# Kernel tuning notes

Measured on AMD Instinct MI355X. Metric: run time of the kernel, lower is better.

The kernel has to match this reference:

```python
import jax, jax.numpy as jnp
import numpy as np
import math

N_HEADS = 16
HEAD_SIZE = 64
N_EMBED = 1024


def setup_inputs() -> dict:
    key = jax.random.key(0)
    ks = jax.random.split(key, 5)
    B, T, C = 2, 2048, N_EMBED
    s = 0.02
    return {
        "x": jax.random.normal(ks[0], (B, T, C), dtype=jnp.float32),
        "c_attn_w": jax.random.normal(ks[1], (C, 3 * C), dtype=jnp.float32) * s,
        "c_attn_b": jax.random.normal(ks[2], (3 * C,), dtype=jnp.float32) * s,
        "c_proj_w": jax.random.normal(ks[3], (C, C), dtype=jnp.float32) * s,
        "c_proj_b": jax.random.normal(ks[4], (C,), dtype=jnp.float32) * s,
    }


def reference(x, c_attn_w, c_attn_b, c_proj_w, c_proj_b):
    B, T, C = x.shape
    H, D = N_HEADS, HEAD_SIZE
    kqv = x @ c_attn_w + c_attn_b                      # [B,T,3C]
    k, q, v = jnp.split(kqv, 3, axis=-1)               # source split order: k, q, v
    k = k.reshape(B, T, H, D).transpose(0, 2, 1, 3)    # [B,H,T,D]
    q = q.reshape(B, T, H, D).transpose(0, 2, 1, 3)
    v = v.reshape(B, T, H, D).transpose(0, 2, 1, 3)
    # NOTE: faithful to source: scores = K @ Q^T (not Q @ K^T)
    wei = jnp.einsum("bhid,bhjd->bhij", k, q) * (1.0 / math.sqrt(D))
    causal = jnp.tril(jnp.ones((T, T), dtype=bool))    # [T,T]
    wei = jnp.where(causal[None, None], wei, -jnp.inf)
    wei = jax.nn.softmax(wei, axis=-1)
    out = jnp.einsum("bhij,bhjd->bhid", wei, v)        # [B,H,T,D]
    out = out.transpose(0, 2, 1, 3).reshape(B, T, C)
    return out @ c_proj_w + c_proj_b
```

## Files before the change

kernel.cpp:

```cpp
#include <hip/hip_runtime.h>
#include <hip/hip_bf16.h>

typedef unsigned short u16;
typedef unsigned int u32;
typedef __attribute__((ext_vector_type(8))) short bf16x8;
typedef __attribute__((ext_vector_type(4))) float f32x4;

#define MFMA_BF16(a, b, c) __builtin_amdgcn_mfma_f32_16x16x32_bf16((a), (b), (c), 0, 0, 0)

__device__ __forceinline__ u16 f2bf(float f) {
    u32 u;
    __builtin_memcpy(&u, &f, 4);
    u += 0x7fffu + ((u >> 16) & 1u);
    return (u16)(u >> 16);
}

__device__ __forceinline__ void glds16(const void* g, void* l) {
    __builtin_amdgcn_global_load_lds(
        (__attribute__((address_space(1))) void*)(g),
        (__attribute__((address_space(3))) void*)(l),
        16, 0, 0);
}

__global__ __launch_bounds__(256) void f32_to_bf16(const float* __restrict__ in,
                                                   u16* __restrict__ out) {
    const int i = blockIdx.x * 256 + threadIdx.x;
    const float4* p = (const float4*)in;
    float4 a = p[i * 2], b = p[i * 2 + 1];
    ushort4 lo, hi;
    lo.x = f2bf(a.x); lo.y = f2bf(a.y); lo.z = f2bf(a.z); lo.w = f2bf(a.w);
    hi.x = f2bf(b.x); hi.y = f2bf(b.y); hi.z = f2bf(b.z); hi.w = f2bf(b.w);
    *(ushort4*)&out[i * 8] = lo;
    *(ushort4*)&out[i * 8 + 4] = hi;
}

__global__ __launch_bounds__(256) void transpose_k(const float* __restrict__ in,
                                                   u16* __restrict__ out,
                                                   int K, int N) {
    __shared__ u16 tl[64][68];
    const int tid = threadIdx.x;
    const int n0 = blockIdx.x * 64, k0 = blockIdx.y * 64;
    #pragma unroll
    for (int it = 0; it < 4; ++it) {
        int idx = tid + it * 256;
        int r = idx >> 4, c4 = (idx & 15) * 4;
        float4 v = *(const float4*)&in[(size_t)(k0 + r) * N + n0 + c4];
        tl[r][c4 + 0] = f2bf(v.x); tl[r][c4 + 1] = f2bf(v.y);
        tl[r][c4 + 2] = f2bf(v.z); tl[r][c4 + 3] = f2bf(v.w);
    }
    __syncthreads();
    #pragma unroll
    for (int it = 0; it < 4; ++it) {
        int idx = tid + it * 256;
        int r = idx >> 4, c4 = (idx & 15) * 4;
        ushort4 v;
        v.x = tl[c4 + 0][r]; v.y = tl[c4 + 1][r];
        v.z = tl[c4 + 2][r]; v.w = tl[c4 + 3][r];
        *(ushort4*)&out[(size_t)(n0 + r) * K + k0 + c4] = v;
    }
}

__global__ __launch_bounds__(256) void transpose_v(const u16* __restrict__ in,
                                                   u16* __restrict__ out) {
    __shared__ u16 tl[64][72];
    const int tid = threadIdx.x;
    const int t0 = blockIdx.x * 64;
    const int bh = blockIdx.y;
    const u16* ip = in + (size_t)bh * 2048 * 64;
    u16* op = out + (size_t)bh * 64 * 2048;
    #pragma unroll
    for (int it = 0; it < 2; ++it) {
        int idx = tid + it * 256;
        int r = idx >> 3, c8 = (idx & 7) * 8;
        *(bf16x8*)&tl[r][c8] = *(const bf16x8*)&ip[(size_t)(t0 + r) * 64 + c8];
    }
    __syncthreads();
    #pragma unroll
    for (int it = 0; it < 2; ++it) {
        int idx = tid + it * 256;
        int d = idx >> 3, c8 = (idx & 7) * 8;
        ushort4 v0, v1;
        v0.x = tl[c8 + 0][d]; v0.y = tl[c8 + 1][d];
        v0.z = tl[c8 + 2][d]; v0.w = tl[c8 + 3][d];
        v1.x = tl[c8 + 4][d]; v1.y = tl[c8 + 5][d];
        v1.z = tl[c8 + 6][d]; v1.w = tl[c8 + 7][d];
        *(ushort4*)&op[(size_t)d * 2048 + t0 + c8] = v0;
        *(ushort4*)&op[(size_t)d * 2048 + t0 + c8 + 4] = v1;
    }
}

__global__ __launch_bounds__(256) void gemm_bt(const u16* __restrict__ A,
                                               const u16* __restrict__ BT,
                                               const float* __restrict__ bias,
                                               u16* __restrict__ out0,
                                               u16* __restrict__ out1,
                                               u16* __restrict__ out2,
                                               float* __restrict__ outf,
                                               int mode) {
    __shared__ u16 As[128 * 32];
    __shared__ u16 Bs[128 * 32];
    const int tid = threadIdx.x;
    const int w = tid >> 6, lane = tid & 63;
    const int c = lane & 15, qd = lane >> 4;
    const int wm = (w >> 1) * 64, wn = (w & 1) * 64;
    const int bm = blockIdx.x * 128, bn = blockIdx.y * 128;
    const int K = 1024;

    f32x4 acc[4][4];
    #pragma unroll
    for (int mt = 0; mt < 4; ++mt)
        #pragma unroll
        for (int nt = 0; nt < 4; ++nt)
            acc[mt][nt] = (f32x4){0.f, 0.f, 0.f, 0.f};

    const u16* aP = A + (size_t)(bm + (tid >> 2)) * K + (tid & 3) * 8;
    const u16* bP = BT + (size_t)(bn + (tid >> 2)) * K + (tid & 3) * 8;
    u16* lA0 = &As[tid * 8];
    u16* lA1 = &As[2048 + tid * 8];
    u16* lB0 = &Bs[tid * 8];
    u16* lB1 = &Bs[2048 + tid * 8];

    for (int kk = 0; kk < K; kk += 32) {
        glds16(aP + kk, lA0);
        glds16(aP + kk + 64 * K, lA1);
        glds16(bP + kk, lB0);
        glds16(bP + kk + 64 * K, lB1);
        __syncthreads();
        bf16x8 af[4], bfr[4];
        #pragma unroll
        for (int mt = 0; mt < 4; ++mt)
            af[mt] = *(const bf16x8*)&As[(wm + mt * 16 + c) * 32 + qd * 8];
        #pragma unroll
        for (int nt = 0; nt < 4; ++nt)
            bfr[nt] = *(const bf16x8*)&Bs[(wn + nt * 16 + c) * 32 + qd * 8];
        #pragma unroll
        for (int mt = 0; mt < 4; ++mt)
            #pragma unroll
            for (int nt = 0; nt < 4; ++nt)
                acc[mt][nt] = MFMA_BF16(af[mt], bfr[nt], acc[mt][nt]);
        __syncthreads();
    }

    #pragma unroll
    for (int nt = 0; nt < 4; ++nt) {
        const int coln = bn + wn + nt * 16 + c;
        const float bv = bias[coln];
        const int reg = coln >> 10;
        const int nr = coln & 1023;
        const int hh = nr >> 6;
        const int dd = nr & 63;
        const float kscl = (mode == 0 && reg == 0) ? 0.18033688f : 1.0f;
        u16* dst = (reg == 0) ? out0 : (reg == 1) ? out1 : out2;
        #pragma unroll
        for (int mt = 0; mt < 4; ++mt) {
            #pragma unroll
            for (int r = 0; r < 4; ++r) {
                const int row = bm + wm + mt * 16 + qd * 4 + r;
                const float ov = (acc[mt][nt][r] + bv) * kscl;
                if (mode == 0) {
                    const int b = row >> 11, t = row & 2047;
                    dst[((b * 16 + hh) * 2048 + t) * 64 + dd] = f2bf(ov);
                } else {
                    outf[(size_t)row * 1024 + coln] = ov;
                }
            }
        }
    }
}

__global__ __launch_bounds__(256, 2) void attn_kernel(const u16* __restrict__ kbuf,
                                                      const u16* __restrict__ qbuf,
                                                      const u16* __restrict__ vtbuf,
                                                      u16* __restrict__ outb) {
    __shared__ __align__(16) u16 Qb[2][64 * 64];
    __shared__ __align__(16) u16 Vb[2][64 * 64];
    __shared__ __align__(16) u16 Ps[4][16 * 72];
    __shared__ float red[4][16];

    const int tid = threadIdx.x;
    const int w = tid >> 6, lane = tid & 63;
    const int c = lane & 15, qd = lane >> 4;
    const int f = blockIdx.x;
    const int g = f >> 3;
    const int bh = (f & 7) * 4 + (g & 3);
    const int pr = g >> 2;
    const u16* kp = kbuf + (size_t)bh * (2048 * 64);
    const u16* qp = qbuf + (size_t)bh * (2048 * 64);
    const u16* vp = vtbuf + (size_t)bh * (64 * 2048);
    const int b = bh >> 4, hh = bh & 15;
    u16* op = outb + (size_t)b * (2048 * 1024) + hh * 64;
    const f32x4 zero4 = {0.f, 0.f, 0.f, 0.f};

    const int slot0 = w * 128 + lane;
    const int slot1 = slot0 + 64;
    const int r0 = slot0 >> 3, r1 = slot1 >> 3;
    const int c8g = ((lane & 7) ^ ((lane >> 3) & 7)) * 8;
    const int swz = (c & 7);

    #pragma unroll
    for (int phase = 0; phase < 2; ++phase) {
        const int ib = (phase == 0) ? pr : 31 - pr;
        const int nj = ib + 1;
        const int iw = ib * 64 + w * 16;

        bf16x8 kf[2];
        #pragma unroll
        for (int kt = 0; kt < 2; ++kt)
            kf[kt] = *(const bf16x8*)&kp[(size_t)(iw + c) * 64 + kt * 32 + qd * 8];

        f32x4 oacc[4];
        #pragma unroll
        for (int nt = 0; nt < 4; ++nt)
            oacc[nt] = zero4;
        float l_lane = 0.f;

        glds16(qp + (size_t)r0 * 64 + c8g, &Qb[0][slot0 * 8]);
        glds16(qp + (size_t)r1 * 64 + c8g, &Qb[0][slot1 * 8]);
        glds16(vp + (size_t)r0 * 2048 + c8g, &Vb[0][slot0 * 8]);
        glds16(vp + (size_t)r1 * 2048 + c8g, &Vb[0][slot1 * 8]);
        __syncthreads();

        for (int jj = 0; jj < nj; ++jj) {
            const int cur = jj & 1;
            if (jj + 1 < nj) {
                const int jn = (jj + 1) * 64;
                const int nb = cur ^ 1;
                glds16(qp + (size_t)(jn + r0) * 64 + c8g, &Qb[nb][slot0 * 8]);
                glds16(qp + (size_t)(jn + r1) * 64 + c8g, &Qb[nb][slot1 * 8]);
                glds16(vp + (size_t)r0 * 2048 + jn + c8g, &Vb[nb][slot0 * 8]);
                glds16(vp + (size_t)r1 * 2048 + jn + c8g, &Vb[nb][slot1 * 8]);
            }
            const int j0 = jj * 64;

            bf16x8 qf[4][2];
            #pragma unroll
            for (int jt = 0; jt < 4; ++jt)
                #pragma unroll
                for (int kt = 0; kt < 2; ++kt)
                    qf[jt][kt] = *(const bf16x8*)&Qb[cur][(jt * 16 + c) * 64 + (((kt * 4 + qd) ^ swz) << 3)];
            f32x4 sacc[4];
            #pragma unroll
            for (int jt = 0; jt < 4; ++jt) {
                f32x4 s0 = zero4;
                s0 = MFMA_BF16(qf[jt][0], kf[0], s0);
                s0 = MFMA_BF16(qf[jt][1], kf[1], s0);
                sacc[jt] = s0;
            }

            if (j0 + 63 > iw) {
                #pragma unroll
                for (int jt = 0; jt < 4; ++jt)
                    #pragma unroll
                    for (int r = 0; r < 4; ++r) {
                        int j = j0 + jt * 16 + qd * 4 + r;
                        int i = iw + c;
                        if (j > i) sacc[jt][r] = -3.0e38f;
                    }
            }

            #pragma unroll
            for (int jt = 0; jt < 4; ++jt) {
                float p0 = exp2f(sacc[jt][0]);
                float p1 = exp2f(sacc[jt][1]);
                float p2 = exp2f(sacc[jt][2]);
                float p3 = exp2f(sacc[jt][3]);
                l_lane += (p0 + p1) + (p2 + p3);
                ushort4 pk;
                pk.x = f2bf(p0); pk.y = f2bf(p1);
                pk.z = f2bf(p2); pk.w = f2bf(p3);
                *(ushort4*)&Ps[w][c * 72 + jt * 16 + qd * 4] = pk;
            }

            #pragma unroll
            for (int kt = 0; kt < 2; ++kt) {
                bf16x8 pf = *(const bf16x8*)&Ps[w][c * 72 + kt * 32 + qd * 8];
                #pragma unroll
                for (int nt = 0; nt < 4; ++nt) {
                    bf16x8 vf = *(const bf16x8*)&Vb[cur][(nt * 16 + c) * 64 + (((kt * 4 + qd) ^ swz) << 3)];
                    oacc[nt] = MFMA_BF16(pf, vf, oacc[nt]);
                }
            }
            __syncthreads();
        }

        float l = l_lane;
        l += __shfl_xor(l, 16);
        l += __shfl_xor(l, 32);
        red[w][c] = l;
        #pragma unroll
        for (int r = 0; r < 4; ++r) {
            const int irow = iw + qd * 4 + r;
            const float inv = 1.0f / red[w][qd * 4 + r];
            #pragma unroll
            for (int nt = 0; nt < 4; ++nt)
                op[(size_t)irow * 1024 + nt * 16 + c] = f2bf(oacc[nt][r] * inv);
        }
        __syncthreads();
    }
}

extern "C" void kernel_launch(void* const* d_in, const int* in_sizes, int n_in,
                              void* d_out, int out_size, void* d_ws, size_t ws_size,
                              hipStream_t stream) {
    const void *px = nullptr, *paw = nullptr, *pab = nullptr, *ppw = nullptr, *ppb = nullptr;
    for (int i = 0; i < n_in; ++i) {
        switch (in_sizes[i]) {
            case 4194304: px  = d_in[i]; break;
            case 3145728: paw = d_in[i]; break;
            case 3072:    pab = d_in[i]; break;
            case 1048576: ppw = d_in[i]; break;
            case 1024:    ppb = d_in[i]; break;
        }
    }
    if (!px || !paw || !pab || !ppw || !ppb) return;

    char* ws = (char*)d_ws;
    u16* kbuf    = (u16*)(ws);
    u16* qbuf    = (u16*)(ws + 8388608);
    u16* vnat    = (u16*)(ws + 16777216);
    u16* vtr     = (u16*)(ws + 25165824);
    u16* wt_attn = (u16*)(ws + 33554432);
    u16* abuf    = (u16*)(ws + 33554432);
    u16* wt_proj = (u16*)(ws + 16777216);
    float* out   = (float*)d_out;
    u16* xb      = (u16*)d_out;

    f32_to_bf16<<<2048, 256, 0, stream>>>((const float*)px, xb);
    transpose_k<<<dim3(48, 16), 256, 0, stream>>>((const float*)paw, wt_attn, 1024, 3072);
    gemm_bt<<<dim3(32, 24), 256, 0, stream>>>(xb, wt_attn, (const float*)pab,
                                              kbuf, qbuf, vnat, nullptr, 0);
    transpose_v<<<dim3(32, 32), 256, 0, stream>>>(vnat, vtr);
    attn_kernel<<<dim3(512), 256, 0, stream>>>(kbuf, qbuf, vtr, abuf);
    transpose_k<<<dim3(16, 16), 256, 0, stream>>>((const float*)ppw, wt_proj, 1024, 1024);
    gemm_bt<<<dim3(32, 8), 256, 0, stream>>>(abuf, wt_proj, (const float*)ppb,
                                             nullptr, nullptr, nullptr, out, 1);
}
```

Measured before the change: 209.4 us.

## Double-buffer and swizzle GEMM tiles, store QKV interleaved, retile projection GEMM

Both GEMMs now double-buffer their LDS tiles so the next k-slice is prefetched while the current one runs, with one barrier per iteration instead of two. Tile columns are XOR-swizzled to reduce LDS bank conflicts. The QKV GEMM writes a row-major [B*T,3072] buffer instead of scattering to per-head layouts, and attention and the V transpose read K/Q/V with a stride of 3072. The projection GEMM uses 128x64 tiles to launch twice as many blocks, at the cost of strided attention loads and lower data reuse per block.

```diff
diff --git a/kernel.cpp b/kernel.cpp
--- a/kernel.cpp
+++ b/kernel.cpp
@@ -60,19 +60,20 @@
     }
 }
 
-__global__ __launch_bounds__(256) void transpose_v(const u16* __restrict__ in,
+__global__ __launch_bounds__(256) void transpose_v(const u16* __restrict__ kqv,
                                                    u16* __restrict__ out) {
     __shared__ u16 tl[64][72];
     const int tid = threadIdx.x;
     const int t0 = blockIdx.x * 64;
     const int bh = blockIdx.y;
-    const u16* ip = in + (size_t)bh * 2048 * 64;
+    const int b = bh >> 4, hh = bh & 15;
+    const u16* ip = kqv + (size_t)b * 2048 * 3072 + 2048 + hh * 64;
     u16* op = out + (size_t)bh * 64 * 2048;
     #pragma unroll
     for (int it = 0; it < 2; ++it) {
         int idx = tid + it * 256;
         int r = idx >> 3, c8 = (idx & 7) * 8;
-        *(bf16x8*)&tl[r][c8] = *(const bf16x8*)&ip[(size_t)(t0 + r) * 64 + c8];
+        *(bf16x8*)&tl[r][c8] = *(const bf16x8*)&ip[(size_t)(t0 + r) * 3072 + c8];
     }
     __syncthreads();
     #pragma unroll
@@ -89,16 +90,12 @@
     }
 }
 
-__global__ __launch_bounds__(256) void gemm_bt(const u16* __restrict__ A,
-                                               const u16* __restrict__ BT,
-                                               const float* __restrict__ bias,
-                                               u16* __restrict__ out0,
-                                               u16* __restrict__ out1,
-                                               u16* __restrict__ out2,
-                                               float* __restrict__ outf,
-                                               int mode) {
-    __shared__ u16 As[128 * 32];
-    __shared__ u16 Bs[128 * 32];
+__global__ __launch_bounds__(256) void gemm_qkv(const u16* __restrict__ A,
+                                                const u16* __restrict__ BT,
+                                                const float* __restrict__ bias,
+                                                u16* __restrict__ out) {
+    __shared__ u16 As[2][128 * 32];
+    __shared__ u16 Bs[2][128 * 32];
     const int tid = threadIdx.x;
     const int w = tid >> 6, lane = tid & 63;
     const int c = lane & 15, qd = lane >> 4;
@@ -113,26 +110,34 @@
         for (int nt = 0; nt < 4; ++nt)
             acc[mt][nt] = (f32x4){0.f, 0.f, 0.f, 0.f};
 
-    const u16* aP = A + (size_t)(bm + (tid >> 2)) * K + (tid & 3) * 8;
-    const u16* bP = BT + (size_t)(bn + (tid >> 2)) * K + (tid & 3) * 8;
-    u16* lA0 = &As[tid * 8];
-    u16* lA1 = &As[2048 + tid * 8];
-    u16* lB0 = &Bs[tid * 8];
-    u16* lB1 = &Bs[2048 + tid * 8];
+    const int srow = tid >> 2;
+    const int schk8 = ((tid & 3) ^ ((tid >> 3) & 3)) * 8;
+    const u16* aP = A + (size_t)(bm + srow) * K + schk8;
+    const u16* bP = BT + (size_t)(bn + srow) * K + schk8;
+    const int rk = (c >> 1) & 3;
+
+    glds16(aP, &As[0][tid * 8]);
+    glds16(aP + 64 * K, &As[0][2048 + tid * 8]);
+    glds16(bP, &Bs[0][tid * 8]);
+    glds16(bP + 64 * K, &Bs[0][2048 + tid * 8]);
+    __syncthreads();
 
     for (int kk = 0; kk < K; kk += 32) {
-        glds16(aP + kk, lA0);
-        glds16(aP + kk + 64 * K, lA1);
-        glds16(bP + kk, lB0);
-        glds16(bP + kk + 64 * K, lB1);
-        __syncthreads();
+        const int cur = (kk >> 5) & 1;
+        if (kk + 32 < K) {
+            const int nb = cur ^ 1;
+            glds16(aP + kk + 32, &As[nb][tid * 8]);
+            glds16(aP + kk + 32 + 64 * K, &As[nb][2048 + tid * 8]);
+            glds16(bP + kk + 32, &Bs[nb][tid * 8]);
+            glds16(bP + kk + 32 + 64 * K, &Bs[nb][2048 + tid * 8]);
+        }
         bf16x8 af[4], bfr[4];
         #pragma unroll
         for (int mt = 0; mt < 4; ++mt)
-            af[mt] = *(const bf16x8*)&As[(wm + mt * 16 + c) * 32 + qd * 8];
-        #pragma unroll
-        for (int nt = 0; nt < 4; ++nt)
-            bfr[nt] = *(const bf16x8*)&Bs[(wn + nt * 16 + c) * 32 + qd * 8];
+            af[mt] = *(const bf16x8*)&As[cur][(wm + mt * 16 + c) * 32 + ((qd ^ rk) << 3)];
+        #pragma unroll
+        for (int nt = 0; nt < 4; ++nt)
+            bfr[nt] = *(const bf16x8*)&Bs[cur][(wn + nt * 16 + c) * 32 + ((qd ^ rk) << 3)];
         #pragma unroll
         for (int mt = 0; mt < 4; ++mt)
             #pragma unroll
@@ -145,31 +150,86 @@
     for (int nt = 0; nt < 4; ++nt) {
         const int coln = bn + wn + nt * 16 + c;
         const float bv = bias[coln];
-        const int reg = coln >> 10;
-        const int nr = coln & 1023;
-        const int hh = nr >> 6;
-        const int dd = nr & 63;
-        const float kscl = (mode == 0 && reg == 0) ? 0.18033688f : 1.0f;
-        u16* dst = (reg == 0) ? out0 : (reg == 1) ? out1 : out2;
-        #pragma unroll
-        for (int mt = 0; mt < 4; ++mt) {
+        const float kscl = (coln < 1024) ? 0.18033688f : 1.0f;
+        #pragma unroll
+        for (int mt = 0; mt < 4; ++mt)
             #pragma unroll
             for (int r = 0; r < 4; ++r) {
                 const int row = bm + wm + mt * 16 + qd * 4 + r;
-                const float ov = (acc[mt][nt][r] + bv) * kscl;
-                if (mode == 0) {
-                    const int b = row >> 11, t = row & 2047;
-                    dst[((b * 16 + hh) * 2048 + t) * 64 + dd] = f2bf(ov);
-                } else {
-                    outf[(size_t)row * 1024 + coln] = ov;
-                }
-            }
-        }
-    }
-}
-
-__global__ __launch_bounds__(256, 2) void attn_kernel(const u16* __restrict__ kbuf,
-                                                      const u16* __restrict__ qbuf,
+                out[(size_t)row * 3072 + coln] = f2bf((acc[mt][nt][r] + bv) * kscl);
+            }
+    }
+}
+
+__global__ __launch_bounds__(256) void gemm_proj(const u16* __restrict__ A,
+                                                 const u16* __restrict__ BT,
+                                                 const float* __restrict__ bias,
+                                                 float* __restrict__ outf) {
+    __shared__ u16 As[2][128 * 32];
+    __shared__ u16 Bs[2][64 * 32];
+    const int tid = threadIdx.x;
+    const int w = tid >> 6, lane = tid & 63;
+    const int c = lane & 15, qd = lane >> 4;
+    const int wm = w * 32;
+    const int bm = blockIdx.x * 128, bn = blockIdx.y * 64;
+    const int K = 1024;
+
+    f32x4 acc[2][4];
+    #pragma unroll
+    for (int mt = 0; mt < 2; ++mt)
+        #pragma unroll
+        for (int nt = 0; nt < 4; ++nt)
+            acc[mt][nt] = (f32x4){0.f, 0.f, 0.f, 0.f};
+
+    const int srow = tid >> 2;
+    const int schk8 = ((tid & 3) ^ ((tid >> 3) & 3)) * 8;
+    const u16* aP = A + (size_t)(bm + srow) * K + schk8;
+    const u16* bP = BT + (size_t)(bn + srow) * K + schk8;
+    const int rk = (c >> 1) & 3;
+
+    glds16(aP, &As[0][tid * 8]);
+    glds16(aP + 64 * K, &As[0][2048 + tid * 8]);
+    glds16(bP, &Bs[0][tid * 8]);
+    __syncthreads();
+
+    for (int kk = 0; kk < K; kk += 32) {
+        const int cur = (kk >> 5) & 1;
+        if (kk + 32 < K) {
+            const int nb = cur ^ 1;
+            glds16(aP + kk + 32, &As[nb][tid * 8]);
+            glds16(aP + kk + 32 + 64 * K, &As[nb][2048 + tid * 8]);
+            glds16(bP + kk + 32, &Bs[nb][tid * 8]);
+        }
+        bf16x8 af[2], bfr[4];
+        #pragma unroll
+        for (int mt = 0; mt < 2; ++mt)
+            af[mt] = *(const bf16x8*)&As[cur][(wm + mt * 16 + c) * 32 + ((qd ^ rk) << 3)];
+        #pragma unroll
+        for (int nt = 0; nt < 4; ++nt)
+            bfr[nt] = *(const bf16x8*)&Bs[cur][(nt * 16 + c) * 32 + ((qd ^ rk) << 3)];
+        #pragma unroll
+        for (int mt = 0; mt < 2; ++mt)
+            #pragma unroll
+            for (int nt = 0; nt < 4; ++nt)
+                acc[mt][nt] = MFMA_BF16(af[mt], bfr[nt], acc[mt][nt]);
+        __syncthreads();
+    }
+
+    #pragma unroll
+    for (int nt = 0; nt < 4; ++nt) {
+        const int coln = bn + nt * 16 + c;
+        const float bv = bias[coln];
+        #pragma unroll
+        for (int mt = 0; mt < 2; ++mt)
+            #pragma unroll
+            for (int r = 0; r < 4; ++r) {
+                const int row = bm + wm + mt * 16 + qd * 4 + r;
+                outf[(size_t)row * 1024 + coln] = acc[mt][nt][r] + bv;
+            }
+    }
+}
+
+__global__ __launch_bounds__(256, 2) void attn_kernel(const u16* __restrict__ kqv,
                                                       const u16* __restrict__ vtbuf,
                                                       u16* __restrict__ outb) {
     __shared__ __align__(16) u16 Qb[2][64 * 64];
@@ -184,10 +244,10 @@
     const int g = f >> 3;
     const int bh = (f & 7) * 4 + (g & 3);
     const int pr = g >> 2;
-    const u16* kp = kbuf + (size_t)bh * (2048 * 64);
-    const u16* qp = qbuf + (size_t)bh * (2048 * 64);
+    const int b = bh >> 4, hh = bh & 15;
+    const u16* kp = kqv + (size_t)b * 2048 * 3072 + hh * 64;
+    const u16* qp = kqv + (size_t)b * 2048 * 3072 + 1024 + hh * 64;
     const u16* vp = vtbuf + (size_t)bh * (64 * 2048);
-    const int b = bh >> 4, hh = bh & 15;
     u16* op = outb + (size_t)b * (2048 * 1024) + hh * 64;
     const f32x4 zero4 = {0.f, 0.f, 0.f, 0.f};
 
@@ -206,7 +266,7 @@
         bf16x8 kf[2];
         #pragma unroll
         for (int kt = 0; kt < 2; ++kt)
-            kf[kt] = *(const bf16x8*)&kp[(size_t)(iw + c) * 64 + kt * 32 + qd * 8];
+            kf[kt] = *(const bf16x8*)&kp[(size_t)(iw + c) * 3072 + kt * 32 + qd * 8];
 
         f32x4 oacc[4];
         #pragma unroll
@@ -214,8 +274,8 @@
             oacc[nt] = zero4;
         float l_lane = 0.f;
 
-        glds16(qp + (size_t)r0 * 64 + c8g, &Qb[0][slot0 * 8]);
-        glds16(qp + (size_t)r1 * 64 + c8g, &Qb[0][slot1 * 8]);
+        glds16(qp + (size_t)r0 * 3072 + c8g, &Qb[0][slot0 * 8]);
+        glds16(qp + (size_t)r1 * 3072 + c8g, &Qb[0][slot1 * 8]);
         glds16(vp + (size_t)r0 * 2048 + c8g, &Vb[0][slot0 * 8]);
         glds16(vp + (size_t)r1 * 2048 + c8g, &Vb[0][slot1 * 8]);
         __syncthreads();
@@ -225,8 +285,8 @@
             if (jj + 1 < nj) {
                 const int jn = (jj + 1) * 64;
                 const int nb = cur ^ 1;
-                glds16(qp + (size_t)(jn + r0) * 64 + c8g, &Qb[nb][slot0 * 8]);
-                glds16(qp + (size_t)(jn + r1) * 64 + c8g, &Qb[nb][slot1 * 8]);
+                glds16(qp + (size_t)(jn + r0) * 3072 + c8g, &Qb[nb][slot0 * 8]);
+                glds16(qp + (size_t)(jn + r1) * 3072 + c8g, &Qb[nb][slot1 * 8]);
                 glds16(vp + (size_t)r0 * 2048 + jn + c8g, &Vb[nb][slot0 * 8]);
                 glds16(vp + (size_t)r1 * 2048 + jn + c8g, &Vb[nb][slot1 * 8]);
             }
@@ -315,23 +375,19 @@
     if (!px || !paw || !pab || !ppw || !ppb) return;
 
     char* ws = (char*)d_ws;
-    u16* kbuf    = (u16*)(ws);
-    u16* qbuf    = (u16*)(ws + 8388608);
-    u16* vnat    = (u16*)(ws + 16777216);
+    u16* kqv     = (u16*)(ws);
     u16* vtr     = (u16*)(ws + 25165824);
     u16* wt_attn = (u16*)(ws + 33554432);
     u16* abuf    = (u16*)(ws + 33554432);
-    u16* wt_proj = (u16*)(ws + 16777216);
+    u16* wt_proj = (u16*)(ws);
     float* out   = (float*)d_out;
     u16* xb      = (u16*)d_out;
 
     f32_to_bf16<<<2048, 256, 0, stream>>>((const float*)px, xb);
     transpose_k<<<dim3(48, 16), 256, 0, stream>>>((const float*)paw, wt_attn, 1024, 3072);
-    gemm_bt<<<dim3(32, 24), 256, 0, stream>>>(xb, wt_attn, (const float*)pab,
-                                              kbuf, qbuf, vnat, nullptr, 0);
-    transpose_v<<<dim3(32, 32), 256, 0, stream>>>(vnat, vtr);
-    attn_kernel<<<dim3(512), 256, 0, stream>>>(kbuf, qbuf, vtr, abuf);
+    gemm_qkv<<<dim3(32, 24), 256, 0, stream>>>(xb, wt_attn, (const float*)pab, kqv);
+    transpose_v<<<dim3(32, 32), 256, 0, stream>>>(kqv, vtr);
+    attn_kernel<<<dim3(512), 256, 0, stream>>>(kqv, vtr, abuf);
     transpose_k<<<dim3(16, 16), 256, 0, stream>>>((const float*)ppw, wt_proj, 1024, 1024);
-    gemm_bt<<<dim3(32, 8), 256, 0, stream>>>(abuf, wt_proj, (const float*)ppb,
-                                             nullptr, nullptr, nullptr, out, 1);
-}
+    gemm_proj<<<dim3(32, 16), 256, 0, stream>>>(abuf, wt_proj, (const float*)ppb, out);
+}
```

Result: faster. 190.8 us (-8.9%).
